# Optimization experiments

Measured on AMD Instinct MI355X. Metric: run time of the kernel, lower is better.

## Reference

```python
import jax, jax.numpy as jnp
import numpy as np

GROUP_SIZE = 128
ZERO_POINT = 8  # symmetric int4 zero point


def setup_inputs() -> dict:
    key = jax.random.key(0)
    k1, k2, k3 = jax.random.split(key, 3)
    M, K, N = 8192, 4096, 4096
    x = jax.random.normal(k1, (M, K), dtype=jnp.float16)
    # logical unpacked int4 codes in [0, 16)
    q_weight = jax.random.randint(k2, (K, N), 0, 16, dtype=jnp.int32)
    # per-group scales, small positive values like real quantized checkpoints
    scale = (jax.random.uniform(k3, (K // GROUP_SIZE, N), dtype=jnp.float32) * 0.02 + 0.001).astype(jnp.float16)
    return {"x": x, "q_weight": q_weight, "scale": scale}


def reference(x, q_weight, scale):
    # Dequantize: w[k, n] = (q[k, n] - zp) * scale[k // group, n]
    K, N = q_weight.shape
    g = K // scale.shape[0]  # group size
    scale_full = jnp.repeat(scale, g, axis=0)  # [K, N]
    w = (q_weight.astype(jnp.float16) - jnp.float16(ZERO_POINT)) * scale_full
    # GEMM with fp32 accumulation, fp16 output (Marlin semantics)
    y = jnp.dot(x, w, preferred_element_type=jnp.float32).astype(jnp.float16)
    return y
```

## Files before the change

kernel.cpp:

```cpp
#include <hip/hip_runtime.h>
#include <stdint.h>
#include <math.h>

#define GROUP 128
#define ZP 8
#define BM 256
#define BN 256
#define BK 32

typedef short short8 __attribute__((ext_vector_type(8)));
typedef float floatx4 __attribute__((ext_vector_type(4)));

typedef __attribute__((address_space(3))) void lds_void;
typedef const __attribute__((address_space(1))) void gbl_void;
#define GLOAD_LDS16(g, l) \
  __builtin_amdgcn_global_load_lds((gbl_void*)(g), (lds_void*)(l), 16, 0, 0)

#define VMCNT(n) asm volatile("s_waitcnt vmcnt(" #n ")" ::: "memory")
#define LGKM0()  asm volatile("s_waitcnt lgkmcnt(0)" ::: "memory")
#define BAR()    __builtin_amdgcn_s_barrier()
#define SCHEDB() __builtin_amdgcn_sched_barrier(0)

__device__ __forceinline__ ushort f2bf(float f) {
    union { float f; uint32_t i; } v; v.f = f;
    uint32_t r = v.i + 0x7FFF + ((v.i >> 16) & 1);
    return (ushort)(r >> 16);
}

__global__ __launch_bounds__(256) void prep_kernel(
    const float* __restrict__ x, const int* __restrict__ q,
    const float* __restrict__ scale, ushort* __restrict__ xb,
    ushort* __restrict__ wt, int K, int N, size_t total8, int ndeq)
{
    __shared__ ushort T[64 * 68];
    const int t = threadIdx.x;

    if ((int)blockIdx.x < ndeq) {
        const int ktiles = K / 64;
        const int k0 = (blockIdx.x % ktiles) * 64;
        const int n0 = (blockIdx.x / ktiles) * 64;
        const int g  = k0 / GROUP;
        const int c  = (t & 15) * 4;
        const int r0 = (t >> 4);

        const float4 s = *reinterpret_cast<const float4*>(&scale[(size_t)g * N + n0 + c]);

#pragma unroll
        for (int j = 0; j < 4; ++j) {
            const int r = r0 + j * 16;
            const int4 qv = *reinterpret_cast<const int4*>(&q[(size_t)(k0 + r) * N + n0 + c]);
            T[(c + 0) * 68 + r] = f2bf((float)(qv.x - ZP) * s.x);
            T[(c + 1) * 68 + r] = f2bf((float)(qv.y - ZP) * s.y);
            T[(c + 2) * 68 + r] = f2bf((float)(qv.z - ZP) * s.z);
            T[(c + 3) * 68 + r] = f2bf((float)(qv.w - ZP) * s.w);
        }
        __syncthreads();
#pragma unroll
        for (int j = 0; j < 4; ++j) {
            const int nn = r0 + j * 16;
            const int kk = c;
            const uint2 v = *reinterpret_cast<const uint2*>(&T[nn * 68 + kk]);
            *reinterpret_cast<uint2*>(&wt[(size_t)(n0 + nn) * K + k0 + kk]) = v;
        }
    } else {
        const size_t nblk   = (size_t)(gridDim.x - ndeq);
        const size_t stride = nblk * 256;
        for (size_t id = (size_t)(blockIdx.x - ndeq) * 256 + t; id < total8; id += stride) {
            const float4 a = *reinterpret_cast<const float4*>(x + id * 8);
            const float4 b = *reinterpret_cast<const float4*>(x + id * 8 + 4);
            ushort o[8] __attribute__((aligned(16)));
            o[0] = f2bf(a.x); o[1] = f2bf(a.y); o[2] = f2bf(a.z); o[3] = f2bf(a.w);
            o[4] = f2bf(b.x); o[5] = f2bf(b.y); o[6] = f2bf(b.z); o[7] = f2bf(b.w);
            *reinterpret_cast<uint4*>(xb + id * 8) = *reinterpret_cast<const uint4*>(o);
        }
    }
}

__global__ __launch_bounds__(512, 2) void gemm256_ring_kernel(
    const ushort* __restrict__ Ab, const ushort* __restrict__ Wt,
    float* __restrict__ out, int M, int N, int K)
{
    __shared__ ushort smem[4 * 16384];

    const int bid = blockIdx.x;
    const int nwg = gridDim.x;
    int wg = bid;
    if ((nwg & 7) == 0) {
        const int cpx = nwg >> 3;
        wg = (bid & 7) * cpx + (bid >> 3);
    }
    const int ntn = N / BN;
    const int m0 = (wg / ntn) * BM;
    const int n0 = (wg % ntn) * BN;

    const int t    = threadIdx.x;
    const int lane = t & 63;
    const int w    = t >> 6;
    const int wm   = w >> 2;
    const int wn   = w & 3;
    const int NT   = K / BK;

    const ushort* pa[2]; const ushort* pb[2];
    int dstA[2], dstB[2];
#pragma unroll
    for (int s = 0; s < 2; ++s) {
        const int r = s * 128 + (t >> 2);
        const int j = (t & 3) ^ ((r >> 1) & 3);
        pa[s] = Ab + (size_t)(m0 + r) * K + j * 8;
        pb[s] = Wt + (size_t)(n0 + r) * K + j * 8;
        dstA[s] = s * 8192 + t * 16;
        dstB[s] = 16384 + s * 8192 + t * 16;
    }

    int aoff[8], boff[4];
#pragma unroll
    for (int i = 0; i < 8; ++i) {
        const int r = wm * 128 + i * 16 + (lane & 15);
        aoff[i] = r * 64 + (((lane >> 4) ^ ((r >> 1) & 3)) << 4);
    }
#pragma unroll
    for (int j = 0; j < 4; ++j) {
        const int r = wn * 64 + j * 16 + (lane & 15);
        boff[j] = 16384 + r * 64 + (((lane >> 4) ^ ((r >> 1) & 3)) << 4);
    }

    floatx4 acc[8][4];
#pragma unroll
    for (int i = 0; i < 8; ++i)
#pragma unroll
        for (int j = 0; j < 4; ++j) acc[i][j] = floatx4{0.f, 0.f, 0.f, 0.f};

#pragma unroll
    for (int U = 0; U < 3; ++U) {
        char* sb = (char*)smem + U * 32768;
        GLOAD_LDS16(pa[0] + U * 32, sb + dstA[0]);
        GLOAD_LDS16(pa[1] + U * 32, sb + dstA[1]);
        GLOAD_LDS16(pb[0] + U * 32, sb + dstB[0]);
        GLOAD_LDS16(pb[1] + U * 32, sb + dstB[1]);
    }
    VMCNT(8);
    BAR();

    auto body = [&](int T, bool issue) __attribute__((always_inline)) {
        if (issue) {
            char* sd = (char*)smem + ((T + 3) & 3) * 32768;
            const int ko = (T + 3) * 32;
            GLOAD_LDS16(pa[0] + ko, sd + dstA[0]);
            GLOAD_LDS16(pa[1] + ko, sd + dstA[1]);
            GLOAD_LDS16(pb[0] + ko, sd + dstB[0]);
            GLOAD_LDS16(pb[1] + ko, sd + dstB[1]);
        }
        const char* sb = (const char*)smem + (T & 3) * 32768;
        short8 af[8], bf[4];
#pragma unroll
        for (int i = 0; i < 8; ++i)
            af[i] = *reinterpret_cast<const short8*>(sb + aoff[i]);
#pragma unroll
        for (int j = 0; j < 4; ++j)
            bf[j] = *reinterpret_cast<const short8*>(sb + boff[j]);
        __builtin_amdgcn_s_setprio(1);
#pragma unroll
        for (int i = 0; i < 8; ++i)
#pragma unroll
            for (int j = 0; j < 4; ++j)
                acc[i][j] = __builtin_amdgcn_mfma_f32_16x16x32_bf16(af[i], bf[j], acc[i][j], 0, 0, 0);
        __builtin_amdgcn_s_setprio(0);
        LGKM0();
        SCHEDB();
    };

    for (int T = 0; T + 3 < NT; ++T) {
        body(T, true);
        VMCNT(8);
        BAR();
    }
    body(NT - 3, false); VMCNT(4); BAR();
    body(NT - 2, false); VMCNT(0); BAR();
    body(NT - 1, false);

    const int orow0 = m0 + wm * 128 + (lane >> 4) * 4;
    const int ocol0 = n0 + wn * 64 + (lane & 15);
#pragma unroll
    for (int i = 0; i < 8; ++i)
#pragma unroll
        for (int j = 0; j < 4; ++j)
#pragma unroll
            for (int r = 0; r < 4; ++r)
                out[(size_t)(orow0 + i * 16 + r) * N + ocol0 + j * 16] = acc[i][j][r];
}

#define MR 16
__global__ __launch_bounds__(256) void naive_kernel(
    const float* __restrict__ x, const int* __restrict__ q,
    const float* __restrict__ sc, float* __restrict__ out,
    int M, int N, int K)
{
    const int n  = blockIdx.x * 256 + threadIdx.x;
    const int m0 = blockIdx.y * MR;
    float acc[MR];
#pragma unroll
    for (int i = 0; i < MR; ++i) acc[i] = 0.f;
    for (int k = 0; k < K; ++k) {
        const float s = sc[(size_t)(k / GROUP) * N + n];
        const float w = (float)(q[(size_t)k * N + n] - ZP) * s;
#pragma unroll
        for (int i = 0; i < MR; ++i)
            acc[i] = fmaf(x[(size_t)(m0 + i) * K + k], w, acc[i]);
    }
#pragma unroll
    for (int i = 0; i < MR; ++i)
        out[(size_t)(m0 + i) * N + n] = acc[i];
}

extern "C" void kernel_launch(void* const* d_in, const int* in_sizes, int n_in,
                              void* d_out, int out_size, void* d_ws, size_t ws_size,
                              hipStream_t stream) {
    const float* x  = (const float*)d_in[0];
    const int*   q  = (const int*)d_in[1];
    const float* sc = (const float*)d_in[2];
    float*       o  = (float*)d_out;

    int M = 8192, K = 4096, N = 4096;
    if (!((long long)in_sizes[0] == (long long)M * K &&
          (long long)in_sizes[1] == (long long)K * N &&
          (long long)out_size    == (long long)M * N)) {
        const double S0 = (double)in_sizes[0], S1 = (double)in_sizes[1];
        K = (int)llround(sqrt(S0 * S1 / (double)out_size));
        N = in_sizes[1] / K;
        M = in_sizes[0] / K;
    }

    const size_t xb_bytes = (size_t)M * K * 2;
    const size_t wt_bytes = (size_t)N * K * 2;

    const bool ok = (M % BM == 0) && (N % BN == 0) && (K % BK == 0) &&
                    (K / BK >= 4) && (N % 64 == 0) && (K % 64 == 0) &&
                    (K % GROUP == 0) && (ws_size >= xb_bytes + wt_bytes);

    if (ok) {
        ushort* xb = (ushort*)d_ws;
        ushort* wt = (ushort*)((char*)d_ws + xb_bytes);
        const int ndeq = (K / 64) * (N / 64);
        prep_kernel<<<dim3(ndeq + 2048), 256, 0, stream>>>(
            x, q, sc, xb, wt, K, N, (size_t)M * K / 8, ndeq);
        const int ngemm = (M / BM) * (N / BN);
        gemm256_ring_kernel<<<dim3(ngemm), 512, 0, stream>>>(xb, wt, o, M, N, K);
    } else {
        naive_kernel<<<dim3(N / 256, M / MR), 256, 0, stream>>>(x, q, sc, o, M, N, K);
    }
}
```

Measured before the change: 291.5 us.

## Software-pipeline LDS fragment reads one K-step ahead of MFMAs

Restructures the GEMM main loop so the LDS reads for the next K-tile are issued right after the current tile's MFMAs, before the barrier, rather than at the start of each iteration. This lets the LDS reads overlap with the barrier wait and the next iteration's global-to-LDS staging. Fragments now stay live in registers across iterations, which raises register pressure. The tail is rewritten to match, and the minimum K-tile count goes from 4 to 5.

```diff
diff --git a/kernel.cpp b/kernel.cpp
--- a/kernel.cpp
+++ b/kernel.cpp
@@ -76,7 +76,7 @@
     }
 }
 
-__global__ __launch_bounds__(512, 2) void gemm256_ring_kernel(
+__global__ __launch_bounds__(512, 2) void gemm256_pipe_kernel(
     const ushort* __restrict__ Ab, const ushort* __restrict__ Wt,
     float* __restrict__ out, int M, int N, int K)
 {
@@ -130,34 +130,26 @@
 #pragma unroll
         for (int j = 0; j < 4; ++j) acc[i][j] = floatx4{0.f, 0.f, 0.f, 0.f};
 
-#pragma unroll
-    for (int U = 0; U < 3; ++U) {
-        char* sb = (char*)smem + U * 32768;
-        GLOAD_LDS16(pa[0] + U * 32, sb + dstA[0]);
-        GLOAD_LDS16(pa[1] + U * 32, sb + dstA[1]);
-        GLOAD_LDS16(pb[0] + U * 32, sb + dstB[0]);
-        GLOAD_LDS16(pb[1] + U * 32, sb + dstB[1]);
-    }
-    VMCNT(8);
-    BAR();
-
-    auto body = [&](int T, bool issue) __attribute__((always_inline)) {
-        if (issue) {
-            char* sd = (char*)smem + ((T + 3) & 3) * 32768;
-            const int ko = (T + 3) * 32;
-            GLOAD_LDS16(pa[0] + ko, sd + dstA[0]);
-            GLOAD_LDS16(pa[1] + ko, sd + dstA[1]);
-            GLOAD_LDS16(pb[0] + ko, sd + dstB[0]);
-            GLOAD_LDS16(pb[1] + ko, sd + dstB[1]);
-        }
+    short8 af[8], bf[4];
+
+    auto stage = [&](int Td) __attribute__((always_inline)) {
+        char* sd = (char*)smem + (Td & 3) * 32768;
+        const int ko = Td * 32;
+        GLOAD_LDS16(pa[0] + ko, sd + dstA[0]);
+        GLOAD_LDS16(pa[1] + ko, sd + dstA[1]);
+        GLOAD_LDS16(pb[0] + ko, sd + dstB[0]);
+        GLOAD_LDS16(pb[1] + ko, sd + dstB[1]);
+    };
+    auto read_frags = [&](int T) __attribute__((always_inline)) {
         const char* sb = (const char*)smem + (T & 3) * 32768;
-        short8 af[8], bf[4];
 #pragma unroll
         for (int i = 0; i < 8; ++i)
             af[i] = *reinterpret_cast<const short8*>(sb + aoff[i]);
 #pragma unroll
         for (int j = 0; j < 4; ++j)
             bf[j] = *reinterpret_cast<const short8*>(sb + boff[j]);
+    };
+    auto mfma_all = [&]() __attribute__((always_inline)) {
         __builtin_amdgcn_s_setprio(1);
 #pragma unroll
         for (int i = 0; i < 8; ++i)
@@ -165,18 +157,28 @@
             for (int j = 0; j < 4; ++j)
                 acc[i][j] = __builtin_amdgcn_mfma_f32_16x16x32_bf16(af[i], bf[j], acc[i][j], 0, 0, 0);
         __builtin_amdgcn_s_setprio(0);
+    };
+
+    stage(0); stage(1); stage(2);
+    VMCNT(4);
+    BAR();
+    read_frags(0);
+
+    for (int T = 0; T + 3 < NT; ++T) {
         LGKM0();
         SCHEDB();
-    };
-
-    for (int T = 0; T + 3 < NT; ++T) {
-        body(T, true);
-        VMCNT(8);
+        stage(T + 3);
+        mfma_all();
+        SCHEDB();
+        VMCNT(4);
+        read_frags(T + 1);
         BAR();
     }
-    body(NT - 3, false); VMCNT(4); BAR();
-    body(NT - 2, false); VMCNT(0); BAR();
-    body(NT - 1, false);
+    LGKM0(); SCHEDB(); mfma_all(); SCHEDB();
+    VMCNT(0); read_frags(NT - 2); BAR();
+    LGKM0(); SCHEDB(); mfma_all();
+    read_frags(NT - 1);
+    LGKM0(); SCHEDB(); mfma_all();
 
     const int orow0 = m0 + wm * 128 + (lane >> 4) * 4;
     const int ocol0 = n0 + wn * 64 + (lane & 15);
@@ -234,7 +236,7 @@
     const size_t wt_bytes = (size_t)N * K * 2;
 
     const bool ok = (M % BM == 0) && (N % BN == 0) && (K % BK == 0) &&
-                    (K / BK >= 4) && (N % 64 == 0) && (K % 64 == 0) &&
+                    (K / BK >= 5) && (N % 64 == 0) && (K % 64 == 0) &&
                     (K % GROUP == 0) && (ws_size >= xb_bytes + wt_bytes);
 
     if (ok) {
@@ -244,7 +246,7 @@
         prep_kernel<<<dim3(ndeq + 2048), 256, 0, stream>>>(
             x, q, sc, xb, wt, K, N, (size_t)M * K / 8, ndeq);
         const int ngemm = (M / BM) * (N / BN);
-        gemm256_ring_kernel<<<dim3(ngemm), 512, 0, stream>>>(xb, wt, o, M, N, K);
+        gemm256_pipe_kernel<<<dim3(ngemm), 512, 0, stream>>>(xb, wt, o, M, N, K);
     } else {
         naive_kernel<<<dim3(N / 256, M / MR), 256, 0, stream>>>(x, q, sc, o, M, N, K);
     }
```

New measurement: 285.2 us. 1.02x faster.
